# Kernel optimization log

Hardware: AMD Instinct MI355X
Metric: run time of the kernel (lower is better)

## Reference

```python
import jax, jax.numpy as jnp
import numpy as np

B, L, D, H, DK, DV = 2, 2048, 1024, 16, 64, 64
NEG_INF = -100000000.0


def setup_inputs() -> dict:
    key = jax.random.key(0)
    ks = jax.random.split(key, 10)
    s = 0.02
    inp = {
        "q": jax.random.normal(ks[0], (B, L, D), jnp.float32),
        "k": jax.random.normal(ks[1], (B, L, D), jnp.float32),
        "v": jax.random.normal(ks[2], (B, L, D), jnp.float32),
        "Wq": jax.random.normal(ks[3], (D, H * DK), jnp.float32) * s,
        "bq": jnp.zeros((H * DK,), jnp.float32),
        "Wk": jax.random.normal(ks[4], (D, H * DK), jnp.float32) * s,
        "bk": jnp.zeros((H * DK,), jnp.float32),
        "Wv": jax.random.normal(ks[5], (D, H * DV), jnp.float32) * s,
        "bv": jnp.zeros((H * DV,), jnp.float32),
        "W0": jax.random.normal(ks[6], (H * DV, D), jnp.float32) * s,
        "b0": jnp.zeros((D,), jnp.float32),
        "key_padding_mask": jax.random.uniform(ks[7], (B, L)) < 0.1,
        # 3D causal mask (B, Lq, Lk); True = masked
        "attn_mask": jnp.broadcast_to(jnp.triu(jnp.ones((L, L), bool), k=1), (B, L, L)),
    }
    return inp


def reference(q, k, v, Wq, bq, Wk, bk, Wv, bv, W0, b0, key_padding_mask, attn_mask):
    b, lq, _ = q.shape
    lk = k.shape[1]
    dk = Wq.shape[1] // H
    dv = Wv.shape[1] // H
    qh = (q @ Wq + bq).reshape(b, lq, H, dk)  # (B,Lq,H,dk)
    kh = (k @ Wk + bk).reshape(b, lk, H, dk)
    vh = (v @ Wv + bv).reshape(b, lk, H, dv)
    # scaled scores (B,H,Lq,Lk)
    attn = jnp.einsum("bqhd,bkhd->bhqk", qh, kh) / jnp.sqrt(jnp.float32(dk))
    # attn_mask (B,Lq,Lk): masked_fill semantics
    attn = jnp.where(attn_mask[:, None, :, :], NEG_INF, attn)
    # key_padding_mask (B,Lq): masks full query rows (broadcast over keys)
    attn = jnp.where(key_padding_mask[:, None, :, None], NEG_INF, attn)
    attn = jax.nn.softmax(attn, axis=-1)
    out = jnp.einsum("bhqk,bkhd->bqhd", attn, vh).reshape(b, lq, H * dv)
    out = out @ W0 + b0  # (B,Lq,D)
    return out, attn
```

## Files before the change

kernel.cpp:

```cpp
#include <hip/hip_runtime.h>

#define B_ 2
#define L_ 2048
#define D_ 1024
#define H_ 16
#define DKV 64
#define NEG_INF -1e8f

typedef float f32x4 __attribute__((ext_vector_type(4)));
typedef __bf16 bf16x8 __attribute__((ext_vector_type(8)));
typedef unsigned int u32x4 __attribute__((ext_vector_type(4)));
typedef unsigned int u32x2 __attribute__((ext_vector_type(2)));
typedef unsigned short u16x4 __attribute__((ext_vector_type(4)));

__device__ __forceinline__ unsigned short f2bfbits(float f) {
  unsigned int u = __builtin_bit_cast(unsigned int, f);
  unsigned int r = (u + 0x7FFFu + ((u >> 16) & 1u)) >> 16;
  return (unsigned short)r;
}
__device__ __forceinline__ float bf2f(unsigned short b) {
  unsigned int u = ((unsigned int)b) << 16;
  return __builtin_bit_cast(float, u);
}

__device__ __forceinline__ void gload16(const unsigned short* g, unsigned short* l) {
  __builtin_amdgcn_global_load_lds(
      (const __attribute__((address_space(1))) unsigned int*)g,
      (__attribute__((address_space(3))) unsigned int*)l, 16, 0, 0);
}

__global__ __launch_bounds__(256) void prep_k(
    const float* __restrict__ xq, const float* __restrict__ xk, const float* __restrict__ xv,
    const float* __restrict__ Wq, const float* __restrict__ Wk,
    const float* __restrict__ Wv, const float* __restrict__ W0,
    const void* __restrict__ kpm_raw,
    unsigned short* __restrict__ oq, unsigned short* __restrict__ ok, unsigned short* __restrict__ ov,
    unsigned short* __restrict__ Wtq, unsigned short* __restrict__ Wtk,
    unsigned short* __restrict__ Wtv, unsigned short* __restrict__ W0t,
    unsigned char* __restrict__ kpmn)
{
  __shared__ float Tl[64][65];
  const int bid = blockIdx.x, tid = threadIdx.x;
  if (bid < 6144) {
    const int proj = bid >> 11;
    const float* X = proj == 0 ? xq : (proj == 1 ? xk : xv);
    unsigned short* O = proj == 0 ? oq : (proj == 1 ? ok : ov);
    const long i8 = ((long)(bid & 2047) * 256 + tid) * 8;
    f32x4 a = *(const f32x4*)(X + i8);
    f32x4 b = *(const f32x4*)(X + i8 + 4);
    u32x4 p;
    p[0] = (unsigned)f2bfbits(a[0]) | ((unsigned)f2bfbits(a[1]) << 16);
    p[1] = (unsigned)f2bfbits(a[2]) | ((unsigned)f2bfbits(a[3]) << 16);
    p[2] = (unsigned)f2bfbits(b[0]) | ((unsigned)f2bfbits(b[1]) << 16);
    p[3] = (unsigned)f2bfbits(b[2]) | ((unsigned)f2bfbits(b[3]) << 16);
    *(u32x4*)(O + i8) = p;
  } else if (bid < 7168) {
    const int wid = bid - 6144;
    const int m = wid >> 8, t = wid & 255;
    const float* W = m == 0 ? Wq : (m == 1 ? Wk : (m == 2 ? Wv : W0));
    unsigned short* Wt = m == 0 ? Wtq : (m == 1 ? Wtk : (m == 2 ? Wtv : W0t));
    const int k0 = ((t >> 4) & 15) * 64, n0 = (t & 15) * 64;
    #pragma unroll
    for (int it = 0; it < 4; ++it) {
      int idx = it * 256 + tid;
      int r = idx >> 4, c4 = (idx & 15) << 2;
      f32x4 x = *(const f32x4*)(W + (long)(k0 + r) * 1024 + n0 + c4);
      Tl[r][c4] = x[0]; Tl[r][c4 + 1] = x[1]; Tl[r][c4 + 2] = x[2]; Tl[r][c4 + 3] = x[3];
    }
    __syncthreads();
    #pragma unroll
    for (int it = 0; it < 2; ++it) {
      int idx = it * 256 + tid;
      int n = idx >> 3, c8 = (idx & 7) << 3;
      u32x4 p;
      #pragma unroll
      for (int j = 0; j < 4; ++j)
        p[j] = (unsigned)f2bfbits(Tl[c8 + 2 * j][n]) | ((unsigned)f2bfbits(Tl[c8 + 2 * j + 1][n]) << 16);
      *(u32x4*)(Wt + (long)(n0 + n) * 1024 + k0 + c8) = p;
    }
  } else {
    __shared__ int flag;
    if (tid == 0) flag = 0;
    __syncthreads();
    const unsigned* w = (const unsigned*)kpm_raw;
    unsigned bad = 0;
    for (int i = tid; i < 1024; i += 256) bad |= (w[i] > 1u) ? 1u : 0u;
    if (bad) flag = 1;
    __syncthreads();
    const bool u8 = (flag != 0);
    const unsigned char* u = (const unsigned char*)kpm_raw;
    for (int i = tid; i < B_ * L_; i += 256)
      kpmn[i] = u8 ? (u[i] != 0) : (w[i] != 0);
  }
}

__global__ __launch_bounds__(256) void colsum_part_k(const unsigned short* __restrict__ vh,
                                                     float* __restrict__ part) {
  __shared__ float red[4][64];
  const int bid = blockIdx.x, tid = threadIdx.x;
  const int z = bid >> 3, seg = bid & 7;
  const int col = tid & 63, rgrp = tid >> 6;
  const long zoff = (long)z * L_ * DKV;
  float s = 0.f;
  #pragma unroll 4
  for (int i = 0; i < 64; ++i) {
    int r = seg * 256 + rgrp + 4 * i;
    s += bf2f(vh[zoff + (long)r * DKV + col]);
  }
  red[rgrp][col] = s;
  __syncthreads();
  if (tid < 64)
    part[(long)bid * 64 + tid] = red[0][tid] + red[1][tid] + red[2][tid] + red[3][tid];
}

__global__ __launch_bounds__(64) void colsum_final_k(const float* __restrict__ part,
                                                     float* __restrict__ colsumV) {
  const int z = blockIdx.x, col = threadIdx.x;
  float s = 0.f;
  #pragma unroll
  for (int seg = 0; seg < 8; ++seg) s += part[((long)z * 8 + seg) * 64 + col];
  colsumV[z * DKV + col] = s;
}

__global__ __launch_bounds__(256) void qkv_gemm_k(
    const unsigned short* __restrict__ xqb, const unsigned short* __restrict__ xkb,
    const unsigned short* __restrict__ xvb,
    const unsigned short* __restrict__ Wtq, const unsigned short* __restrict__ Wtk,
    const unsigned short* __restrict__ Wtv,
    const float* __restrict__ bq, const float* __restrict__ bk, const float* __restrict__ bv,
    unsigned short* __restrict__ oq, unsigned short* __restrict__ ok, unsigned short* __restrict__ ov)
{
  __shared__ __align__(16) unsigned short Al[128][64];
  __shared__ __align__(16) unsigned short Bl[128][64];
  const int proj = blockIdx.y;
  const unsigned short* X  = proj == 0 ? xqb : (proj == 1 ? xkb : xvb);
  const unsigned short* Wt = proj == 0 ? Wtq : (proj == 1 ? Wtk : Wtv);
  const float* bias = proj == 0 ? bq : (proj == 1 ? bk : bv);
  unsigned short* O = proj == 0 ? oq : (proj == 1 ? ok : ov);
  const int mt = blockIdx.x, zp = blockIdx.z;
  const int bb = zp >> 3, hp = zp & 7;
  const int tid = threadIdx.x, lane = tid & 63, w = tid >> 6, g = lane >> 4, l16 = lane & 15;
  const int wm = w >> 1, wn = w & 1;
  const long arow0 = (long)bb * L_ + mt * 128;
  const long brow0 = (long)hp * 128;
  const int lr8 = lane >> 3, lc = lane & 7;

  const f32x4 zero4 = {0.f, 0.f, 0.f, 0.f};
  f32x4 acc[4][4];
  #pragma unroll
  for (int i = 0; i < 4; ++i)
    #pragma unroll
    for (int j = 0; j < 4; ++j) acc[i][j] = zero4;

  for (int kt = 0; kt < D_; kt += 64) {
    #pragma unroll
    for (int i = 0; i < 4; ++i) {
      int r = w * 32 + i * 8 + lr8;
      gload16(X + (arow0 + r) * D_ + kt + ((lc ^ (r & 7)) << 3), &Al[w * 32 + i * 8][0]);
      gload16(Wt + (brow0 + r) * D_ + kt + ((lc ^ (r & 7)) << 3), &Bl[w * 32 + i * 8][0]);
    }
    __syncthreads();
    #pragma unroll
    for (int ks = 0; ks < 2; ++ks) {
      bf16x8 a[4], bv8[4];
      #pragma unroll
      for (int fm = 0; fm < 4; ++fm) {
        int ra = wm * 64 + fm * 16 + l16;
        a[fm] = *(const bf16x8*)&Al[ra][((ks * 4 + g) ^ (ra & 7)) << 3];
      }
      #pragma unroll
      for (int fn = 0; fn < 4; ++fn) {
        int rb = wn * 64 + fn * 16 + l16;
        bv8[fn] = *(const bf16x8*)&Bl[rb][((ks * 4 + g) ^ (rb & 7)) << 3];
      }
      #pragma unroll
      for (int fm = 0; fm < 4; ++fm)
        #pragma unroll
        for (int fn = 0; fn < 4; ++fn)
          acc[fm][fn] = __builtin_amdgcn_mfma_f32_16x16x32_bf16(a[fm], bv8[fn], acc[fm][fn], 0, 0, 0);
    }
    __syncthreads();
  }
  #pragma unroll
  for (int fm = 0; fm < 4; ++fm)
    #pragma unroll
    for (int fn = 0; fn < 4; ++fn)
      #pragma unroll
      for (int r = 0; r < 4; ++r) {
        int row = mt * 128 + wm * 64 + fm * 16 + g * 4 + r;
        int col = wn * 64 + fn * 16 + l16;
        float val = acc[fm][fn][r] + bias[hp * 128 + col];
        int zh = bb * H_ + hp * 2 + (col >> 6);
        O[(long)zh * L_ * 64 + (long)row * 64 + (col & 63)] = f2bfbits(val);
      }
}

__global__ __launch_bounds__(256) void oproj_gemm_k(
    const unsigned short* __restrict__ Ab, const unsigned short* __restrict__ W0t,
    const float* __restrict__ b0, float* __restrict__ out)
{
  __shared__ __align__(16) unsigned short Al[64][64];
  __shared__ __align__(16) unsigned short Bl[128][64];
  const int mt = blockIdx.x, nt = blockIdx.y;
  const int tid = threadIdx.x, lane = tid & 63, w = tid >> 6, g = lane >> 4, l16 = lane & 15;
  const int wm = w >> 1, wn = w & 1;
  const int lr8 = lane >> 3, lc = lane & 7;

  const f32x4 zero4 = {0.f, 0.f, 0.f, 0.f};
  f32x4 acc[2][4];
  #pragma unroll
  for (int i = 0; i < 2; ++i)
    #pragma unroll
    for (int j = 0; j < 4; ++j) acc[i][j] = zero4;

  for (int kt = 0; kt < D_; kt += 64) {
    #pragma unroll
    for (int i = 0; i < 2; ++i) {
      int r = w * 16 + i * 8 + lr8;
      gload16(Ab + (long)(mt * 64 + r) * D_ + kt + ((lc ^ (r & 7)) << 3), &Al[w * 16 + i * 8][0]);
    }
    #pragma unroll
    for (int i = 0; i < 4; ++i) {
      int r = w * 32 + i * 8 + lr8;
      gload16(W0t + (long)(nt * 128 + r) * D_ + kt + ((lc ^ (r & 7)) << 3), &Bl[w * 32 + i * 8][0]);
    }
    __syncthreads();
    #pragma unroll
    for (int ks = 0; ks < 2; ++ks) {
      bf16x8 a[2], bv8[4];
      #pragma unroll
      for (int fm = 0; fm < 2; ++fm) {
        int ra = wm * 32 + fm * 16 + l16;
        a[fm] = *(const bf16x8*)&Al[ra][((ks * 4 + g) ^ (ra & 7)) << 3];
      }
      #pragma unroll
      for (int fn = 0; fn < 4; ++fn) {
        int rb = wn * 64 + fn * 16 + l16;
        bv8[fn] = *(const bf16x8*)&Bl[rb][((ks * 4 + g) ^ (rb & 7)) << 3];
      }
      #pragma unroll
      for (int fm = 0; fm < 2; ++fm)
        #pragma unroll
        for (int fn = 0; fn < 4; ++fn)
          acc[fm][fn] = __builtin_amdgcn_mfma_f32_16x16x32_bf16(a[fm], bv8[fn], acc[fm][fn], 0, 0, 0);
    }
    __syncthreads();
  }
  #pragma unroll
  for (int fm = 0; fm < 2; ++fm)
    #pragma unroll
    for (int fn = 0; fn < 4; ++fn)
      #pragma unroll
      for (int r = 0; r < 4; ++r) {
        int row = mt * 64 + wm * 32 + fm * 16 + g * 4 + r;
        int col = nt * 128 + wn * 64 + fn * 16 + l16;
        out[(long)row * D_ + col] = acc[fm][fn][r] + b0[col];
      }
}

__global__ __launch_bounds__(256, 4) void attn_pv_k(
    const unsigned short* __restrict__ qh, const unsigned short* __restrict__ kh,
    const unsigned short* __restrict__ vh, const unsigned char* __restrict__ kpm,
    const float* __restrict__ colsumV, float* __restrict__ attn,
    unsigned short* __restrict__ oh)
{
  __shared__ __align__(16) char smem[64 * 68 * 4];
  auto Ql = (unsigned short (*)[72])smem;
  auto Pl = (float (*)[68])smem;
  __shared__ __align__(16) unsigned short Kl[64][72];
  __shared__ __align__(16) unsigned short Vl[64][72];
  __shared__ unsigned char padl[64];

  const int tid = threadIdx.x, lane = tid & 63, w = tid >> 6, g = lane >> 4, l16 = lane & 15;
  const int bid = blockIdx.x;
  const int z = bid & 31;
  const int qq5 = bid >> 5;
  const int sx = (qq5 & 8) ? ((qq5 & 16) ? 55 - qq5 : 23 - qq5) : qq5;
  const int q0 = sx * 64;
  const int b = z >> 4, h = z & 15;
  const long zoff = (long)z * L_ * DKV;
  const int rowbase = q0 + w * 16 + g * 4;

  const int kr = tid >> 3, kc8 = (tid & 7) << 3;
  const int vk = tid >> 4, vn4 = (tid & 15) << 2;

  #pragma unroll
  for (int it = 0; it < 2; ++it) {
    int f = it * 256 + tid;
    int r = f >> 3, c8 = (f & 7) << 3;
    *(u32x4*)&Ql[r][c8] = *(const u32x4*)(qh + zoff + (long)(q0 + r) * 64 + c8);
  }
  if (tid < 64) padl[tid] = kpm[b * L_ + q0 + tid];
  __syncthreads();
  bf16x8 a[2];
  #pragma unroll
  for (int ks = 0; ks < 2; ++ks)
    a[ks] = *(const bf16x8*)&Ql[w * 16 + l16][ks * 32 + g * 8];
  bool pad[4];
  #pragma unroll
  for (int r = 0; r < 4; ++r) pad[r] = padl[w * 16 + g * 4 + r] != 0;
  __syncthreads();

  const float invL = 1.0f / (float)L_;

  for (int kt = sx + 1; kt < L_ / 64; ++kt) {
    #pragma unroll
    for (int it = 0; it < 4; ++it) {
      int f = it * 256 + tid;
      int r = f >> 4, c4 = (f & 15) << 2;
      float vvv = padl[r] ? invL : 0.f;
      f32x4 ov = {vvv, vvv, vvv, vvv};
      __builtin_nontemporal_store(ov, (f32x4*)&attn[((long)z * L_ + q0 + r) * L_ + kt * 64 + c4]);
    }
  }

  float psum[4] = {0.f, 0.f, 0.f, 0.f};
  const f32x4 zero4 = {0.f, 0.f, 0.f, 0.f};
  f32x4 o[4];
  #pragma unroll
  for (int fn = 0; fn < 4; ++fn) o[fn] = zero4;

  u32x4 Kreg[2];
  u16x4 Vreg[4];
  #pragma unroll
  for (int it = 0; it < 2; ++it)
    Kreg[it] = *(const u32x4*)(kh + zoff + (long)(kr + it * 32) * 64 + kc8);
  #pragma unroll
  for (int it = 0; it < 4; ++it)
    Vreg[it] = *(const u16x4*)(vh + zoff + (long)(vk + it * 16) * 64 + vn4);

  for (int kt = 0; kt <= sx; ++kt) {
    #pragma unroll
    for (int it = 0; it < 2; ++it)
      *(u32x4*)&Kl[kr + it * 32][kc8] = Kreg[it];
    #pragma unroll
    for (int it = 0; it < 4; ++it) {
      int kk = vk + it * 16;
      int sw = kk ^ (((vn4 >> 2) & 7) << 3);
      Vl[vn4 + 0][sw] = Vreg[it][0]; Vl[vn4 + 1][sw] = Vreg[it][1];
      Vl[vn4 + 2][sw] = Vreg[it][2]; Vl[vn4 + 3][sw] = Vreg[it][3];
    }
    __syncthreads();
    if (kt < sx) {
      const long noff = zoff + (long)((kt + 1) * 64) * 64;
      #pragma unroll
      for (int it = 0; it < 2; ++it)
        Kreg[it] = *(const u32x4*)(kh + noff + (long)(kr + it * 32) * 64 + kc8);
      #pragma unroll
      for (int it = 0; it < 4; ++it)
        Vreg[it] = *(const u16x4*)(vh + noff + (long)(vk + it * 16) * 64 + vn4);
    }
    f32x4 s[4];
    #pragma unroll
    for (int fn = 0; fn < 4; ++fn) {
      bf16x8 bv0 = *(const bf16x8*)&Kl[fn * 16 + l16][g * 8];
      bf16x8 bv1 = *(const bf16x8*)&Kl[fn * 16 + l16][32 + g * 8];
      f32x4 t = zero4;
      t = __builtin_amdgcn_mfma_f32_16x16x32_bf16(a[0], bv0, t, 0, 0, 0);
      t = __builtin_amdgcn_mfma_f32_16x16x32_bf16(a[1], bv1, t, 0, 0, 0);
      s[fn] = t;
    }
    #pragma unroll
    for (int fn = 0; fn < 4; ++fn)
      #pragma unroll
      for (int r = 0; r < 4; ++r) {
        int kk = kt * 64 + fn * 16 + l16;
        float sv = s[fn][r] * 0.125f;
        if (kk > rowbase + r) sv = NEG_INF;
        float p = __expf(sv - 12.0f);
        psum[r] += p;
        Pl[w * 16 + g * 4 + r][fn * 16 + l16] = p;
      }
    bf16x8 pa[2];
    #pragma unroll
    for (int ks = 0; ks < 2; ++ks) {
      f32x4 lo = *(const f32x4*)&Pl[w * 16 + l16][ks * 32 + g * 8];
      f32x4 hi = *(const f32x4*)&Pl[w * 16 + l16][ks * 32 + g * 8 + 4];
      bf16x8 t;
      #pragma unroll
      for (int i = 0; i < 4; ++i) { t[i] = (__bf16)lo[i]; t[i + 4] = (__bf16)hi[i]; }
      pa[ks] = t;
    }
    #pragma unroll
    for (int fn = 0; fn < 4; ++fn) {
      int dv = fn * 16 + l16;
      int swz = ((dv >> 2) & 7) << 3;
      bf16x8 vb0 = *(const bf16x8*)&Vl[dv][(0 * 32 + g * 8) ^ swz];
      bf16x8 vb1 = *(const bf16x8*)&Vl[dv][(1 * 32 + g * 8) ^ swz];
      o[fn] = __builtin_amdgcn_mfma_f32_16x16x32_bf16(pa[0], vb0, o[fn], 0, 0, 0);
      o[fn] = __builtin_amdgcn_mfma_f32_16x16x32_bf16(pa[1], vb1, o[fn], 0, 0, 0);
    }
    __syncthreads();
  }

  float linv[4];
  #pragma unroll
  for (int r = 0; r < 4; ++r) {
    float s = psum[r];
    #pragma unroll
    for (int d = 1; d < 16; d <<= 1) s += __shfl_xor(s, d);
    linv[r] = 1.f / s;
  }

  #pragma unroll
  for (int fn = 0; fn < 4; ++fn)
    #pragma unroll
    for (int r = 0; r < 4; ++r) {
      int qq = rowbase + r;
      int dv = fn * 16 + l16;
      float val = pad[r] ? invL * colsumV[z * DKV + dv] : o[fn][r] * linv[r];
      oh[((long)b * L_ + qq) * (H_ * DKV) + h * DKV + dv] = f2bfbits(val);
    }

  u32x4 K2reg[2];
  #pragma unroll
  for (int it = 0; it < 2; ++it)
    Kreg[it] = *(const u32x4*)(kh + zoff + (long)(kr + it * 32) * 64 + kc8);
  if (1 <= sx)
    #pragma unroll
    for (int it = 0; it < 2; ++it)
      K2reg[it] = *(const u32x4*)(kh + zoff + (long)(64 + kr + it * 32) * 64 + kc8);

  for (int kt = 0; kt <= sx; kt += 2) {
    const bool has2 = (kt + 1 <= sx);
    #pragma unroll
    for (int it = 0; it < 2; ++it)
      *(u32x4*)&Kl[kr + it * 32][kc8] = Kreg[it];
    if (has2)
      #pragma unroll
      for (int it = 0; it < 2; ++it)
        *(u32x4*)&Vl[kr + it * 32][kc8] = K2reg[it];
    __syncthreads();
    if (kt + 2 <= sx) {
      const long noff = zoff + (long)((kt + 2) * 64) * 64;
      #pragma unroll
      for (int it = 0; it < 2; ++it)
        Kreg[it] = *(const u32x4*)(kh + noff + (long)(kr + it * 32) * 64 + kc8);
      if (kt + 3 <= sx)
        #pragma unroll
        for (int it = 0; it < 2; ++it)
          K2reg[it] = *(const u32x4*)(kh + noff + (long)(64 + kr + it * 32) * 64 + kc8);
    }
    #pragma unroll
    for (int fn = 0; fn < 4; ++fn) {
      bf16x8 bv0 = *(const bf16x8*)&Kl[fn * 16 + l16][g * 8];
      bf16x8 bv1 = *(const bf16x8*)&Kl[fn * 16 + l16][32 + g * 8];
      f32x4 t = zero4;
      t = __builtin_amdgcn_mfma_f32_16x16x32_bf16(a[0], bv0, t, 0, 0, 0);
      t = __builtin_amdgcn_mfma_f32_16x16x32_bf16(a[1], bv1, t, 0, 0, 0);
      #pragma unroll
      for (int r = 0; r < 4; ++r) {
        int kk = kt * 64 + fn * 16 + l16;
        float sv = t[r] * 0.125f;
        if (kk > rowbase + r) sv = NEG_INF;
        float p = pad[r] ? invL : __expf(sv - 12.0f) * linv[r];
        Pl[w * 16 + g * 4 + r][fn * 16 + l16] = p;
      }
    }
    __syncthreads();
    #pragma unroll
    for (int it = 0; it < 4; ++it) {
      int f = it * 256 + tid;
      int r = f >> 4, c4 = (f & 15) << 2;
      f32x4 ov = *(const f32x4*)&Pl[r][c4];
      __builtin_nontemporal_store(ov, (f32x4*)&attn[((long)z * L_ + q0 + r) * L_ + kt * 64 + c4]);
    }
    if (has2) {
      __syncthreads();
      #pragma unroll
      for (int fn = 0; fn < 4; ++fn) {
        bf16x8 bv0 = *(const bf16x8*)&Vl[fn * 16 + l16][g * 8];
        bf16x8 bv1 = *(const bf16x8*)&Vl[fn * 16 + l16][32 + g * 8];
        f32x4 t = zero4;
        t = __builtin_amdgcn_mfma_f32_16x16x32_bf16(a[0], bv0, t, 0, 0, 0);
        t = __builtin_amdgcn_mfma_f32_16x16x32_bf16(a[1], bv1, t, 0, 0, 0);
        #pragma unroll
        for (int r = 0; r < 4; ++r) {
          int kk = (kt + 1) * 64 + fn * 16 + l16;
          float sv = t[r] * 0.125f;
          if (kk > rowbase + r) sv = NEG_INF;
          float p = pad[r] ? invL : __expf(sv - 12.0f) * linv[r];
          Pl[w * 16 + g * 4 + r][fn * 16 + l16] = p;
        }
      }
      __syncthreads();
      #pragma unroll
      for (int it = 0; it < 4; ++it) {
        int f = it * 256 + tid;
        int r = f >> 4, c4 = (f & 15) << 2;
        f32x4 ov = *(const f32x4*)&Pl[r][c4];
        __builtin_nontemporal_store(ov, (f32x4*)&attn[((long)z * L_ + q0 + r) * L_ + (kt + 1) * 64 + c4]);
      }
    }
  }
}

extern "C" void kernel_launch(void* const* d_in, const int* in_sizes, int n_in,
                              void* d_out, int out_size, void* d_ws, size_t ws_size,
                              hipStream_t stream) {
  (void)in_sizes; (void)n_in; (void)out_size; (void)ws_size;
  const float* q  = (const float*)d_in[0];
  const float* k  = (const float*)d_in[1];
  const float* v  = (const float*)d_in[2];
  const float* Wq = (const float*)d_in[3];
  const float* bq = (const float*)d_in[4];
  const float* Wk = (const float*)d_in[5];
  const float* bk = (const float*)d_in[6];
  const float* Wv = (const float*)d_in[7];
  const float* bv = (const float*)d_in[8];
  const float* W0 = (const float*)d_in[9];
  const float* b0 = (const float*)d_in[10];
  const void*  kpm_raw = d_in[11];

  float* out  = (float*)d_out;
  float* attn = out + (long)B_ * L_ * D_;

  const long XE = (long)B_ * L_ * D_;
  const long HEAD_ELEMS = (long)B_ * H_ * L_ * DKV;
  unsigned short* qh  = (unsigned short*)d_ws;
  unsigned short* kh  = qh + HEAD_ELEMS;
  unsigned short* vh  = kh + HEAD_ELEMS;
  unsigned short* xqb = vh + HEAD_ELEMS;
  unsigned short* xkb = xqb + XE;
  unsigned short* xvb = xkb + XE;
  unsigned short* oh  = xqb;
  unsigned short* Wtq = xvb + XE;
  unsigned short* Wtk = Wtq + (long)D_ * D_;
  unsigned short* Wtv = Wtk + (long)D_ * D_;
  unsigned short* W0t = Wtv + (long)D_ * D_;
  float* colsumV = (float*)(W0t + (long)D_ * D_);
  float* part    = colsumV + 32 * 64;
  unsigned char* kpmn = (unsigned char*)(part + 256 * 64);

  dim3 blk(256);

  prep_k<<<dim3(7169), blk, 0, stream>>>(
      q, k, v, Wq, Wk, Wv, W0, kpm_raw,
      xqb, xkb, xvb, Wtq, Wtk, Wtv, W0t, kpmn);

  qkv_gemm_k<<<dim3(L_ / 128, 3, B_ * (H_ / 2)), blk, 0, stream>>>(
      xqb, xkb, xvb, Wtq, Wtk, Wtv, bq, bk, bv, qh, kh, vh);

  colsum_part_k<<<dim3(256), blk, 0, stream>>>(vh, part);
  colsum_final_k<<<dim3(32), dim3(64), 0, stream>>>(part, colsumV);

  attn_pv_k<<<dim3(1024), blk, 0, stream>>>(
      qh, kh, vh, kpmn, colsumV, attn, oh);

  oproj_gemm_k<<<dim3(B_ * L_ / 64, D_ / 128), blk, 0, stream>>>(
      oh, W0t, b0, out);
}
```

Measured before the change: 244.3 us.

## Fuse V column-sum into QKV GEMM and stream K via swizzled direct loads

Removes the two colsum kernels and instead reduces the V-projection accumulators inside the QKV GEMM epilogue, writing per-tile partial sums that the attention kernel adds up at start. K tiles are now loaded straight into an XOR-swizzled LDS buffer with gload16 rather than staged through registers, which frees registers and drops padding. The softmax normalisation is folded into the exponent through a log bias, saving a multiply per element. The aim is fewer launches and less register pressure, at the cost of a slightly different colsum (fp32 accumulators instead of bf16-rounded values) and reliance on the async-load helper's correctness.

```diff
diff --git a/kernel.cpp b/kernel.cpp
--- a/kernel.cpp
+++ b/kernel.cpp
@@ -94,41 +94,14 @@
   }
 }
 
-__global__ __launch_bounds__(256) void colsum_part_k(const unsigned short* __restrict__ vh,
-                                                     float* __restrict__ part) {
-  __shared__ float red[4][64];
-  const int bid = blockIdx.x, tid = threadIdx.x;
-  const int z = bid >> 3, seg = bid & 7;
-  const int col = tid & 63, rgrp = tid >> 6;
-  const long zoff = (long)z * L_ * DKV;
-  float s = 0.f;
-  #pragma unroll 4
-  for (int i = 0; i < 64; ++i) {
-    int r = seg * 256 + rgrp + 4 * i;
-    s += bf2f(vh[zoff + (long)r * DKV + col]);
-  }
-  red[rgrp][col] = s;
-  __syncthreads();
-  if (tid < 64)
-    part[(long)bid * 64 + tid] = red[0][tid] + red[1][tid] + red[2][tid] + red[3][tid];
-}
-
-__global__ __launch_bounds__(64) void colsum_final_k(const float* __restrict__ part,
-                                                     float* __restrict__ colsumV) {
-  const int z = blockIdx.x, col = threadIdx.x;
-  float s = 0.f;
-  #pragma unroll
-  for (int seg = 0; seg < 8; ++seg) s += part[((long)z * 8 + seg) * 64 + col];
-  colsumV[z * DKV + col] = s;
-}
-
 __global__ __launch_bounds__(256) void qkv_gemm_k(
     const unsigned short* __restrict__ xqb, const unsigned short* __restrict__ xkb,
     const unsigned short* __restrict__ xvb,
     const unsigned short* __restrict__ Wtq, const unsigned short* __restrict__ Wtk,
     const unsigned short* __restrict__ Wtv,
     const float* __restrict__ bq, const float* __restrict__ bk, const float* __restrict__ bv,
-    unsigned short* __restrict__ oq, unsigned short* __restrict__ ok, unsigned short* __restrict__ ov)
+    unsigned short* __restrict__ oq, unsigned short* __restrict__ ok, unsigned short* __restrict__ ov,
+    float* __restrict__ part)
 {
   __shared__ __align__(16) unsigned short Al[128][64];
   __shared__ __align__(16) unsigned short Bl[128][64];
@@ -193,6 +166,29 @@
         int zh = bb * H_ + hp * 2 + (col >> 6);
         O[(long)zh * L_ * 64 + (long)row * 64 + (col & 63)] = f2bfbits(val);
       }
+
+  if (proj == 2) {
+    float* red = (float*)&Al[0][0];
+    __syncthreads();
+    #pragma unroll
+    for (int fn = 0; fn < 4; ++fn) {
+      float s = 0.f;
+      #pragma unroll
+      for (int fm = 0; fm < 4; ++fm)
+        #pragma unroll
+        for (int r = 0; r < 4; ++r) s += acc[fm][fn][r];
+      red[(wm * 4 + g) * 128 + wn * 64 + fn * 16 + l16] = s;
+    }
+    __syncthreads();
+    if (tid < 128) {
+      float s = 0.f;
+      #pragma unroll
+      for (int i = 0; i < 8; ++i) s += red[i * 128 + tid];
+      s += 128.f * bias[hp * 128 + tid];
+      int zh = bb * H_ + hp * 2 + (tid >> 6);
+      part[((long)zh * 16 + mt) * 64 + (tid & 63)] = s;
+    }
+  }
 }
 
 __global__ __launch_bounds__(256) void oproj_gemm_k(
@@ -261,15 +257,16 @@
 __global__ __launch_bounds__(256, 4) void attn_pv_k(
     const unsigned short* __restrict__ qh, const unsigned short* __restrict__ kh,
     const unsigned short* __restrict__ vh, const unsigned char* __restrict__ kpm,
-    const float* __restrict__ colsumV, float* __restrict__ attn,
+    const float* __restrict__ part, float* __restrict__ attn,
     unsigned short* __restrict__ oh)
 {
   __shared__ __align__(16) char smem[64 * 68 * 4];
   auto Ql = (unsigned short (*)[72])smem;
   auto Pl = (float (*)[68])smem;
-  __shared__ __align__(16) unsigned short Kl[64][72];
+  __shared__ __align__(16) unsigned short Kl[64][64];
   __shared__ __align__(16) unsigned short Vl[64][72];
   __shared__ unsigned char padl[64];
+  __shared__ float csVl[64];
 
   const int tid = threadIdx.x, lane = tid & 63, w = tid >> 6, g = lane >> 4, l16 = lane & 15;
   const int bid = blockIdx.x;
@@ -281,6 +278,7 @@
   const long zoff = (long)z * L_ * DKV;
   const int rowbase = q0 + w * 16 + g * 4;
 
+  const int lr8 = lane >> 3, lc = lane & 7;
   const int kr = tid >> 3, kc8 = (tid & 7) << 3;
   const int vk = tid >> 4, vn4 = (tid & 15) << 2;
 
@@ -290,7 +288,13 @@
     int r = f >> 3, c8 = (f & 7) << 3;
     *(u32x4*)&Ql[r][c8] = *(const u32x4*)(qh + zoff + (long)(q0 + r) * 64 + c8);
   }
-  if (tid < 64) padl[tid] = kpm[b * L_ + q0 + tid];
+  if (tid < 64) {
+    padl[tid] = kpm[b * L_ + q0 + tid];
+    float s = 0.f;
+    #pragma unroll
+    for (int m = 0; m < 16; ++m) s += part[((long)z * 16 + m) * 64 + tid];
+    csVl[tid] = s;
+  }
   __syncthreads();
   bf16x8 a[2];
   #pragma unroll
@@ -320,19 +324,18 @@
   #pragma unroll
   for (int fn = 0; fn < 4; ++fn) o[fn] = zero4;
 
-  u32x4 Kreg[2];
   u16x4 Vreg[4];
-  #pragma unroll
-  for (int it = 0; it < 2; ++it)
-    Kreg[it] = *(const u32x4*)(kh + zoff + (long)(kr + it * 32) * 64 + kc8);
   #pragma unroll
   for (int it = 0; it < 4; ++it)
     Vreg[it] = *(const u16x4*)(vh + zoff + (long)(vk + it * 16) * 64 + vn4);
 
   for (int kt = 0; kt <= sx; ++kt) {
-    #pragma unroll
-    for (int it = 0; it < 2; ++it)
-      *(u32x4*)&Kl[kr + it * 32][kc8] = Kreg[it];
+    const unsigned short* kbase = kh + zoff + (long)(kt * 64) * 64;
+    #pragma unroll
+    for (int i = 0; i < 2; ++i) {
+      int r = w * 16 + i * 8 + lr8;
+      gload16(kbase + (long)r * 64 + ((lc ^ (r & 7)) << 3), &Kl[w * 16 + i * 8][0]);
+    }
     #pragma unroll
     for (int it = 0; it < 4; ++it) {
       int kk = vk + it * 16;
@@ -344,17 +347,15 @@
     if (kt < sx) {
       const long noff = zoff + (long)((kt + 1) * 64) * 64;
       #pragma unroll
-      for (int it = 0; it < 2; ++it)
-        Kreg[it] = *(const u32x4*)(kh + noff + (long)(kr + it * 32) * 64 + kc8);
-      #pragma unroll
       for (int it = 0; it < 4; ++it)
         Vreg[it] = *(const u16x4*)(vh + noff + (long)(vk + it * 16) * 64 + vn4);
     }
     f32x4 s[4];
     #pragma unroll
     for (int fn = 0; fn < 4; ++fn) {
-      bf16x8 bv0 = *(const bf16x8*)&Kl[fn * 16 + l16][g * 8];
-      bf16x8 bv1 = *(const bf16x8*)&Kl[fn * 16 + l16][32 + g * 8];
+      int fk = fn * 16 + l16;
+      bf16x8 bv0 = *(const bf16x8*)&Kl[fk][(g ^ (fk & 7)) << 3];
+      bf16x8 bv1 = *(const bf16x8*)&Kl[fk][((4 + g) ^ (fk & 7)) << 3];
       f32x4 t = zero4;
       t = __builtin_amdgcn_mfma_f32_16x16x32_bf16(a[0], bv0, t, 0, 0, 0);
       t = __builtin_amdgcn_mfma_f32_16x16x32_bf16(a[1], bv1, t, 0, 0, 0);
@@ -393,13 +394,14 @@
     __syncthreads();
   }
 
-  float linv[4];
+  float linv[4], lbias[4];
   #pragma unroll
   for (int r = 0; r < 4; ++r) {
     float s = psum[r];
     #pragma unroll
     for (int d = 1; d < 16; d <<= 1) s += __shfl_xor(s, d);
     linv[r] = 1.f / s;
+    lbias[r] = __logf(linv[r]) - 12.0f;
   }
 
   #pragma unroll
@@ -408,14 +410,11 @@
     for (int r = 0; r < 4; ++r) {
       int qq = rowbase + r;
       int dv = fn * 16 + l16;
-      float val = pad[r] ? invL * colsumV[z * DKV + dv] : o[fn][r] * linv[r];
+      float val = pad[r] ? invL * csVl[dv] : o[fn][r] * linv[r];
       oh[((long)b * L_ + qq) * (H_ * DKV) + h * DKV + dv] = f2bfbits(val);
     }
 
   u32x4 K2reg[2];
-  #pragma unroll
-  for (int it = 0; it < 2; ++it)
-    Kreg[it] = *(const u32x4*)(kh + zoff + (long)(kr + it * 32) * 64 + kc8);
   if (1 <= sx)
     #pragma unroll
     for (int it = 0; it < 2; ++it)
@@ -423,28 +422,26 @@
 
   for (int kt = 0; kt <= sx; kt += 2) {
     const bool has2 = (kt + 1 <= sx);
-    #pragma unroll
-    for (int it = 0; it < 2; ++it)
-      *(u32x4*)&Kl[kr + it * 32][kc8] = Kreg[it];
+    const unsigned short* kbase = kh + zoff + (long)(kt * 64) * 64;
+    #pragma unroll
+    for (int i = 0; i < 2; ++i) {
+      int r = w * 16 + i * 8 + lr8;
+      gload16(kbase + (long)r * 64 + ((lc ^ (r & 7)) << 3), &Kl[w * 16 + i * 8][0]);
+    }
     if (has2)
       #pragma unroll
       for (int it = 0; it < 2; ++it)
         *(u32x4*)&Vl[kr + it * 32][kc8] = K2reg[it];
     __syncthreads();
-    if (kt + 2 <= sx) {
-      const long noff = zoff + (long)((kt + 2) * 64) * 64;
+    if (kt + 3 <= sx)
       #pragma unroll
       for (int it = 0; it < 2; ++it)
-        Kreg[it] = *(const u32x4*)(kh + noff + (long)(kr + it * 32) * 64 + kc8);
-      if (kt + 3 <= sx)
-        #pragma unroll
-        for (int it = 0; it < 2; ++it)
-          K2reg[it] = *(const u32x4*)(kh + noff + (long)(64 + kr + it * 32) * 64 + kc8);
-    }
+        K2reg[it] = *(const u32x4*)(kh + zoff + (long)((kt + 3) * 64 + kr + it * 32) * 64 + kc8);
     #pragma unroll
     for (int fn = 0; fn < 4; ++fn) {
-      bf16x8 bv0 = *(const bf16x8*)&Kl[fn * 16 + l16][g * 8];
-      bf16x8 bv1 = *(const bf16x8*)&Kl[fn * 16 + l16][32 + g * 8];
+      int fk = fn * 16 + l16;
+      bf16x8 bv0 = *(const bf16x8*)&Kl[fk][(g ^ (fk & 7)) << 3];
+      bf16x8 bv1 = *(const bf16x8*)&Kl[fk][((4 + g) ^ (fk & 7)) << 3];
       f32x4 t = zero4;
       t = __builtin_amdgcn_mfma_f32_16x16x32_bf16(a[0], bv0, t, 0, 0, 0);
       t = __builtin_amdgcn_mfma_f32_16x16x32_bf16(a[1], bv1, t, 0, 0, 0);
@@ -452,8 +449,7 @@
       for (int r = 0; r < 4; ++r) {
         int kk = kt * 64 + fn * 16 + l16;
         float sv = t[r] * 0.125f;
-        if (kk > rowbase + r) sv = NEG_INF;
-        float p = pad[r] ? invL : __expf(sv - 12.0f) * linv[r];
+        float p = pad[r] ? invL : __expf((kk > rowbase + r) ? NEG_INF : (sv + lbias[r]));
         Pl[w * 16 + g * 4 + r][fn * 16 + l16] = p;
       }
     }
@@ -478,8 +474,7 @@
         for (int r = 0; r < 4; ++r) {
           int kk = (kt + 1) * 64 + fn * 16 + l16;
           float sv = t[r] * 0.125f;
-          if (kk > rowbase + r) sv = NEG_INF;
-          float p = pad[r] ? invL : __expf(sv - 12.0f) * linv[r];
+          float p = pad[r] ? invL : __expf((kk > rowbase + r) ? NEG_INF : (sv + lbias[r]));
           Pl[w * 16 + g * 4 + r][fn * 16 + l16] = p;
         }
       }
@@ -528,9 +523,8 @@
   unsigned short* Wtk = Wtq + (long)D_ * D_;
   unsigned short* Wtv = Wtk + (long)D_ * D_;
   unsigned short* W0t = Wtv + (long)D_ * D_;
-  float* colsumV = (float*)(W0t + (long)D_ * D_);
-  float* part    = colsumV + 32 * 64;
-  unsigned char* kpmn = (unsigned char*)(part + 256 * 64);
+  float* part = (float*)(W0t + (long)D_ * D_);
+  unsigned char* kpmn = (unsigned char*)(part + 32 * 16 * 64);
 
   dim3 blk(256);
 
@@ -539,13 +533,10 @@
       xqb, xkb, xvb, Wtq, Wtk, Wtv, W0t, kpmn);
 
   qkv_gemm_k<<<dim3(L_ / 128, 3, B_ * (H_ / 2)), blk, 0, stream>>>(
-      xqb, xkb, xvb, Wtq, Wtk, Wtv, bq, bk, bv, qh, kh, vh);
-
-  colsum_part_k<<<dim3(256), blk, 0, stream>>>(vh, part);
-  colsum_final_k<<<dim3(32), dim3(64), 0, stream>>>(part, colsumV);
+      xqb, xkb, xvb, Wtq, Wtk, Wtv, bq, bk, bv, qh, kh, vh, part);
 
   attn_pv_k<<<dim3(1024), blk, 0, stream>>>(
-      qh, kh, vh, kpmn, colsumV, attn, oh);
+      qh, kh, vh, kpmn, part, attn, oh);
 
   oproj_gemm_k<<<dim3(B_ * L_ / 64, D_ / 128), blk, 0, stream>>>(
       oh, W0t, b0, out);
```

Result: faster. 238.6 us (-2.3%).
